# Performance work log

Measured on AMD Instinct MI355X. Metric: run time of the kernel, lower is better.

The kernel has to match this reference:

```python
import jax, jax.numpy as jnp
import numpy as np

N = 2048
D_T = 256; D_F = 256
E_T = 32; E_F = 32; E_C = 128
C = 5; Q = 512


def setup_inputs() -> dict:
    key = jax.random.key(0)
    ks = jax.random.split(key, 12)
    # full graph minus self-loops, row-major (matches dense_to_sparse ordering)
    r, c = np.meshgrid(np.arange(N), np.arange(N), indexing='ij')
    m = r != c
    edge_index = jnp.asarray(np.stack([r[m], c[m]]), dtype=jnp.int32)  # [2, N*(N-1)]
    E = edge_index.shape[1]
    s = 0.02
    return {
        'time_features': jax.random.normal(ks[0], (N, D_T), jnp.float32),
        'edge_index': edge_index,
        'time_edge_weight': jax.random.uniform(ks[1], (E,), jnp.float32),
        'freq_features': jax.random.normal(ks[2], (N, D_F), jnp.float32),
        'freq_edge_weight': jax.random.uniform(ks[3], (E,), jnp.float32),
        'labels': jax.random.randint(ks[4], (N,), 0, C, jnp.int32),
        'num_classes': C,
        'query_size': Q,
        'Wt': jax.random.normal(ks[5], (D_T, E_T), jnp.float32) * s,
        'bt': jnp.zeros((E_T,), jnp.float32),
        'Wf': jax.random.normal(ks[6], (D_F, E_F), jnp.float32) * s,
        'bf': jnp.zeros((E_F,), jnp.float32),
        'Wc': jax.random.normal(ks[7], (E_T + E_F + C, E_C), jnp.float32) * s,
        'bc': jnp.zeros((E_C,), jnp.float32),
        'Wo': jax.random.normal(ks[8], (E_C, C), jnp.float32) * s,
        'bo': jnp.zeros((C,), jnp.float32),
    }


def _gcn(x, A, W, b):
    # torch_geometric GCNConv: D^{-1/2}(A + I)D^{-1/2} (X W) + b
    n = A.shape[0]
    Ah = A + jnp.eye(n, dtype=A.dtype)
    deg = Ah.sum(axis=1)
    dis = jnp.where(deg > 0, jax.lax.rsqrt(deg), 0.0)
    return (dis[:, None] * Ah * dis[None, :]) @ (x @ W) + b


def reference(time_features, edge_index, time_edge_weight, freq_features,
              freq_edge_weight, labels, num_classes, query_size,
              Wt, bt, Wf, bf, Wc, bc, Wo, bo):
    n = time_features.shape[0]
    lrelu = lambda z: jax.nn.leaky_relu(z, 0.01)

    def dense_adj(w):  # A[dst, src] = w
        return jnp.zeros((n, n), w.dtype).at[edge_index[1], edge_index[0]].add(w)

    te = lrelu(_gcn(time_features, dense_adj(time_edge_weight), Wt, bt))
    fe = lrelu(_gcn(freq_features, dense_adj(freq_edge_weight), Wf, bf))

    # to_one_hot: one_hot[:n - query_size, labels] = 1 -> support rows get 1 in
    # every column that appears anywhere in `labels`
    cols = jnp.zeros((num_classes,), te.dtype).at[labels].set(1.0)
    rowmask = (jnp.arange(n) < (n - query_size)).astype(te.dtype)
    one_hot = rowmask[:, None] * cols[None, :]

    feats = jnp.concatenate([te, fe, one_hot], axis=-1)  # [n, E_T+E_F+C]

    # graph_construction (no_grad in original): 1 / (L1 distance over the
    # non-one-hot dims + 1e-5), zero diagonal
    fd = jax.lax.stop_gradient(feats[:, : feats.shape[1] - num_classes])
    dist = jnp.sum(jnp.abs(fd[:, None, :] - fd[None, :, :]), axis=-1)  # [n, n]
    Aw = (1.0 / (dist + 1e-5)) * (1.0 - jnp.eye(n, dtype=feats.dtype))

    emb = lrelu(_gcn(feats, Aw, Wc, bc))
    return emb @ Wo + bo
```

## Files before the change

kernel.cpp:

```cpp
#include <hip/hip_runtime.h>
#include <hip/hip_bf16.h>

#define N 2048
#define NM1 2047
#define DT 256
#define ET 32
#define EC 128
#define NC 5
#define FS 80
#define FD 69
#define KC_ET 16
#define KC_EC 16

typedef __hip_bfloat16 bf16;

__global__ __launch_bounds__(256) void k_deg_label(const float* __restrict__ tw,
                                                   const float* __restrict__ fw,
                                                   const int* __restrict__ labels,
                                                   float* __restrict__ degT,
                                                   float* __restrict__ degF,
                                                   float* __restrict__ cols){
    int b = blockIdx.x;
    int t = threadIdx.x;
    if (b == 512){
        __shared__ float lc[NC];
        if (t < NC) lc[t] = 0.f;
        __syncthreads();
        for (int i = t; i < N; i += 256){
            int l = labels[i];
            if (l >= 0 && l < NC) lc[l] = 1.f;
        }
        __syncthreads();
        if (t < NC) cols[t] = lc[t];
        return;
    }
    int p = (b & 7)*256 + t;
    if (p >= NM1) return;
    int s0 = (b >> 3)*32;
    float lowT=0.f, highT=0.f, lowF=0.f, highF=0.f;
    #pragma unroll 8
    for (int r = 0; r < 32; ++r){
        int s = s0 + r;
        float vt = tw[(size_t)s*NM1 + p];
        float vf = fw[(size_t)s*NM1 + p];
        if (s <= p){ highT += vt; highF += vf; }
        else       { lowT  += vt; lowF  += vf; }
    }
    atomicAdd(&degT[p],   lowT);
    atomicAdd(&degF[p],   lowF);
    atomicAdd(&degT[p+1], highT);
    atomicAdd(&degF[p+1], highF);
}

__global__ __launch_bounds__(256) void k_xw2(const float* __restrict__ Xt,
                                             const float* __restrict__ Wt,
                                             const float* __restrict__ degT,
                                             float* __restrict__ Zt,
                                             const float* __restrict__ Xf,
                                             const float* __restrict__ Wf,
                                             const float* __restrict__ degF,
                                             float* __restrict__ Zf){
    const float* X   = blockIdx.y ? Xf   : Xt;
    const float* W   = blockIdx.y ? Wf   : Wt;
    const float* deg = blockIdx.y ? degF : degT;
    float*       Z   = blockIdx.y ? Zf   : Zt;
    __shared__ float Ws[DT*ET];
    __shared__ float Xs[8*DT];
    int t = threadIdx.x;
    for (int idx = t; idx < DT*ET; idx += 256) Ws[idx] = W[idx];
    int i0 = blockIdx.x*8;
    for (int idx = t; idx < 8*DT; idx += 256) Xs[idx] = X[(size_t)i0*DT + idx];
    __syncthreads();
    int r = t >> 5, f = t & 31;
    const float* xr = Xs + r*DT;
    float acc = 0.f;
    #pragma unroll 8
    for (int d = 0; d < DT; ++d) acc += xr[d]*Ws[d*ET+f];
    int i = i0 + r;
    Z[(size_t)i*ET+f] = rsqrtf(1.f + deg[i])*acc;
}

__global__ __launch_bounds__(128) void k_agg_et(const float* __restrict__ tw,
                                                const float* __restrict__ fw,
                                                const float* __restrict__ Zt,
                                                const float* __restrict__ Zf,
                                                float* __restrict__ Pt,
                                                float* __restrict__ Pf){
    __shared__ float Ast[64*68];
    __shared__ float Asf[64*68];
    __shared__ float Zst[64*ET];
    __shared__ float Zsf[64*ET];
    int t = threadIdx.x;
    int i0 = blockIdx.x*64;
    int kc = blockIdx.y;
    int k0 = kc*128;
    int rowg = t >> 3;
    int colth = t & 7;
    int r0 = rowg*4, c0 = colth*4;
    float accT[4][4], accF[4][4];
    #pragma unroll
    for (int u=0;u<4;++u)
        #pragma unroll
        for (int v=0;v<4;++v){ accT[u][v]=0.f; accF[u][v]=0.f; }

    for (int kt = 0; kt < 2; ++kt){
        int kb = k0 + kt*64;
        #pragma unroll
        for (int e = 0; e < 32; ++e){
            int id = t + e*128;
            int k_l = id >> 6, i_l = id & 63;
            int k = kb + k_l;
            int gi = i0 + i_l;
            float vt, vf;
            if (gi == k){ vt = 0.f; vf = 0.f; }
            else {
                size_t base = (size_t)k*NM1 + gi - (gi > k ? 1 : 0);
                vt = tw[base]; vf = fw[base];
            }
            Ast[k_l*68 + i_l] = vt;
            Asf[k_l*68 + i_l] = vf;
        }
        #pragma unroll
        for (int e = 0; e < 4; ++e){
            int id = t + e*128;
            int row = id >> 3;
            int c4  = (id & 7)*4;
            *(float4*)&Zst[row*ET + c4] = *(const float4*)&Zt[(size_t)(kb+row)*ET + c4];
            *(float4*)&Zsf[row*ET + c4] = *(const float4*)&Zf[(size_t)(kb+row)*ET + c4];
        }
        __syncthreads();
        for (int k = 0; k < 64; ++k){
            float4 at = *(const float4*)&Ast[k*68 + r0];
            float4 af = *(const float4*)&Asf[k*68 + r0];
            float4 zt = *(const float4*)&Zst[k*ET + c0];
            float4 zf = *(const float4*)&Zsf[k*ET + c0];
            const float* ap = (const float*)&at;
            const float* bp = (const float*)&af;
            const float* zp = (const float*)&zt;
            const float* wp = (const float*)&zf;
            #pragma unroll
            for (int u = 0; u < 4; ++u)
                #pragma unroll
                for (int v = 0; v < 4; ++v){
                    accT[u][v] += ap[u]*zp[v];
                    accF[u][v] += bp[u]*wp[v];
                }
        }
        __syncthreads();
    }
    #pragma unroll
    for (int u = 0; u < 4; ++u){
        size_t ii = (size_t)(i0 + r0 + u);
        float4 ot, of;
        float* pt = (float*)&ot; float* pf = (float*)&of;
        #pragma unroll
        for (int v = 0; v < 4; ++v){ pt[v]=accT[u][v]; pf[v]=accF[u][v]; }
        *(float4*)&Pt[(size_t)kc*(N*ET) + ii*ET + c0] = ot;
        *(float4*)&Pf[(size_t)kc*(N*ET) + ii*ET + c0] = of;
    }
}

__global__ __launch_bounds__(256) void k_feats_epi(const float* __restrict__ Pt,
                                                   const float* __restrict__ Pf,
                                                   const float* __restrict__ Zt,
                                                   const float* __restrict__ Zf,
                                                   const float* __restrict__ degT,
                                                   const float* __restrict__ degF,
                                                   const float* __restrict__ bt,
                                                   const float* __restrict__ bfv,
                                                   const float* __restrict__ cols,
                                                   const int* __restrict__ qsize,
                                                   float* __restrict__ feats){
    int idx = blockIdx.x*256 + threadIdx.x;
    int i = idx >> 6;
    int f = idx & 63;
    float s, rd, b;
    if (f < ET){
        s = Zt[(size_t)i*ET + f];
        #pragma unroll
        for (int kc = 0; kc < KC_ET; ++kc) s += Pt[(size_t)kc*(N*ET) + (size_t)i*ET + f];
        rd = rsqrtf(1.f + degT[i]);
        b = bt[f];
    } else {
        int g = f - ET;
        s = Zf[(size_t)i*ET + g];
        #pragma unroll
        for (int kc = 0; kc < KC_ET; ++kc) s += Pf[(size_t)kc*(N*ET) + (size_t)i*ET + g];
        rd = rsqrtf(1.f + degF[i]);
        b = bfv[g];
    }
    float v = rd*s + b;
    feats[(size_t)i*FS + f] = v > 0.f ? v : 0.01f*v;
    if (f < NC){
        int nsup = N - qsize[0];
        feats[(size_t)i*FS + 2*ET + f] = (i < nsup) ? cols[f] : 0.f;
    }
}

__global__ __launch_bounds__(256) void k_build_aw(const float* __restrict__ feats,
                                                  float* __restrict__ Aw,
                                                  float* __restrict__ dsum){
    __shared__ float fiT[64*68];
    __shared__ float fjT[64*68];
    int t = threadIdx.x;
    int i0 = blockIdx.x*64, j0 = blockIdx.y*64;
    {
        int row = t >> 2;
        int cb  = (t & 3)*16;
        const float4* si = (const float4*)(feats + (size_t)(i0+row)*FS + cb);
        const float4* sj = (const float4*)(feats + (size_t)(j0+row)*FS + cb);
        #pragma unroll
        for (int s = 0; s < 4; ++s){
            float4 v = si[s];
            float4 w = sj[s];
            int c = cb + s*4;
            fiT[(c+0)*68+row]=v.x; fiT[(c+1)*68+row]=v.y; fiT[(c+2)*68+row]=v.z; fiT[(c+3)*68+row]=v.w;
            fjT[(c+0)*68+row]=w.x; fjT[(c+1)*68+row]=w.y; fjT[(c+2)*68+row]=w.z; fjT[(c+3)*68+row]=w.w;
        }
    }
    __syncthreads();
    int tx = t & 15, ty = t >> 4;
    float acc[4][4];
    #pragma unroll
    for (int u=0;u<4;++u)
        #pragma unroll
        for (int v=0;v<4;++v) acc[u][v]=0.f;
    for (int d = 0; d < 64; ++d){
        float4 a4 = *(const float4*)&fiT[d*68 + ty*4];
        float4 b4 = *(const float4*)&fjT[d*68 + tx*4];
        const float* ap = (const float*)&a4;
        const float* bp = (const float*)&b4;
        #pragma unroll
        for (int u = 0; u < 4; ++u)
            #pragma unroll
            for (int v = 0; v < 4; ++v)
                acc[u][v] += fabsf(ap[u]-bp[v]);
    }
    #pragma unroll
    for (int u = 0; u < 4; ++u){
        int gi = i0 + ty*4 + u;
        float4 o;
        float* po = (float*)&o;
        #pragma unroll
        for (int v = 0; v < 4; ++v){
            int gj = j0 + tx*4 + v;
            po[v] = (gi==gj) ? 1.0f : 1.0f/(acc[u][v] + 1e-5f);
        }
        *(float4*)&Aw[(size_t)gi*N + j0 + tx*4] = o;
        float rs = (po[0]+po[1]) + (po[2]+po[3]);
        rs += __shfl_xor(rs, 1);
        rs += __shfl_xor(rs, 2);
        rs += __shfl_xor(rs, 4);
        rs += __shfl_xor(rs, 8);
        if (tx == 0) atomicAdd(&dsum[gi], rs);
    }
}

__global__ __launch_bounds__(256) void k_featswc(const float* __restrict__ feats,
                                                 const float* __restrict__ Wc,
                                                 const float* __restrict__ dsum,
                                                 float* __restrict__ Zc){
    __shared__ float Wcs[FD*EC];
    __shared__ float fr[8][FD+3];
    int t = threadIdx.x;
    for (int idx = t; idx < FD*EC; idx += 256) Wcs[idx] = Wc[idx];
    int i0 = blockIdx.x*8;
    for (int idx = t; idx < 8*FD; idx += 256){
        int r = idx / FD;
        int c = idx - r*FD;
        fr[r][c] = feats[(size_t)(i0+r)*FS + c];
    }
    __syncthreads();
    int f  = t & 127;
    int rh = t >> 7;
    for (int rr = 0; rr < 4; ++rr){
        int r = rh*4 + rr;
        float acc = 0.f;
        #pragma unroll
        for (int d = 0; d < FD; ++d) acc += fr[r][d]*Wcs[d*EC+f];
        int i = i0 + r;
        Zc[(size_t)i*EC + f] = rsqrtf(dsum[i])*acc;
    }
}

__global__ __launch_bounds__(128) void k_agg_ec(const float* __restrict__ Aw,
                                                const float* __restrict__ Zc,
                                                float* __restrict__ Pe){
    __shared__ float AwT[64*68];
    __shared__ float Zs[64*132];
    int t = threadIdx.x;
    int i0 = blockIdx.x*64;
    int kc = blockIdx.y;
    int k0 = kc*128;
    int colth = t & 15, rowg = t >> 4;
    int r0 = rowg*8, c0 = colth*8;
    float acc[8][8];
    #pragma unroll
    for (int u=0;u<8;++u)
        #pragma unroll
        for (int v=0;v<8;++v) acc[u][v]=0.f;

    for (int kt = 0; kt < 2; ++kt){
        int kb = k0 + kt*64;
        #pragma unroll
        for (int e = 0; e < 8; ++e){
            int id = t + e*128;
            int i_l = id >> 4;
            int k4  = (id & 15)*4;
            float4 v = *(const float4*)&Aw[(size_t)(i0+i_l)*N + kb + k4];
            AwT[(k4+0)*68 + i_l] = v.x;
            AwT[(k4+1)*68 + i_l] = v.y;
            AwT[(k4+2)*68 + i_l] = v.z;
            AwT[(k4+3)*68 + i_l] = v.w;
        }
        #pragma unroll
        for (int e = 0; e < 16; ++e){
            int id = t + e*128;
            int row = id >> 5;
            int c4  = (id & 31)*4;
            *(float4*)&Zs[row*132 + c4] = *(const float4*)&Zc[(size_t)(kb+row)*EC + c4];
        }
        __syncthreads();
        for (int k = 0; k < 64; ++k){
            float4 alo = *(const float4*)&AwT[k*68 + r0];
            float4 ahi = *(const float4*)&AwT[k*68 + r0 + 4];
            float4 zlo = *(const float4*)&Zs[k*132 + c0];
            float4 zhi = *(const float4*)&Zs[k*132 + c0 + 4];
            float a8[8] = {alo.x,alo.y,alo.z,alo.w,ahi.x,ahi.y,ahi.z,ahi.w};
            float z8[8] = {zlo.x,zlo.y,zlo.z,zlo.w,zhi.x,zhi.y,zhi.z,zhi.w};
            #pragma unroll
            for (int u = 0; u < 8; ++u)
                #pragma unroll
                for (int v = 0; v < 8; ++v)
                    acc[u][v] += a8[u]*z8[v];
        }
        __syncthreads();
    }
    #pragma unroll
    for (int u = 0; u < 8; ++u){
        size_t ii = (size_t)(i0 + r0 + u);
        float4 o0, o1;
        float* p0 = (float*)&o0; float* p1 = (float*)&o1;
        #pragma unroll
        for (int v = 0; v < 4; ++v){ p0[v]=acc[u][v]; p1[v]=acc[u][v+4]; }
        *(float4*)&Pe[(size_t)kc*(N*EC) + ii*EC + c0]     = o0;
        *(float4*)&Pe[(size_t)kc*(N*EC) + ii*EC + c0 + 4] = o1;
    }
}

__global__ __launch_bounds__(256) void k_emb_epi(const float* __restrict__ Pe,
                                                 const float* __restrict__ dsum,
                                                 const float* __restrict__ bc,
                                                 float* __restrict__ emb){
    int idx = blockIdx.x*256 + threadIdx.x;
    int i = idx >> 7, f = idx & 127;
    float s = 0.f;
    #pragma unroll
    for (int kc = 0; kc < KC_EC; ++kc) s += Pe[(size_t)kc*(N*EC) + (size_t)idx];
    float v = rsqrtf(dsum[i])*s + bc[f];
    emb[idx] = v > 0.f ? v : 0.01f*v;
}

__global__ __launch_bounds__(256) void k_final(const float* __restrict__ emb,
                                               const float* __restrict__ Wo,
                                               const float* __restrict__ bo,
                                               float* __restrict__ out){
    __shared__ float Wos[EC*NC];
    __shared__ float bos[NC];
    int t = threadIdx.x;
    for (int idx = t; idx < EC*NC; idx += 256) Wos[idx] = Wo[idx];
    if (t < NC) bos[t] = bo[t];
    __syncthreads();
    int idx = blockIdx.x*256 + t;
    int i = idx / NC;
    int c = idx - i*NC;
    float acc = bos[c];
    const float* er = emb + (size_t)i*EC;
    #pragma unroll 8
    for (int f = 0; f < EC; ++f) acc += er[f]*Wos[f*NC+c];
    out[idx] = acc;
}

extern "C" void kernel_launch(void* const* d_in, const int* in_sizes, int n_in,
                              void* d_out, int out_size, void* d_ws, size_t ws_size,
                              hipStream_t stream) {
    const float* time_features = (const float*)d_in[0];
    const float* tw            = (const float*)d_in[2];
    const float* freq_features = (const float*)d_in[3];
    const float* fw            = (const float*)d_in[4];
    const int*   labels        = (const int*)d_in[5];
    const int*   qsize         = (const int*)d_in[7];
    const float* Wt  = (const float*)d_in[8];
    const float* bt  = (const float*)d_in[9];
    const float* Wf  = (const float*)d_in[10];
    const float* bfv = (const float*)d_in[11];
    const float* Wc  = (const float*)d_in[12];
    const float* bc  = (const float*)d_in[13];
    const float* Wo  = (const float*)d_in[14];
    const float* bo  = (const float*)d_in[15];
    float* out = (float*)d_out;

    float* ws    = (float*)d_ws;
    float* Zt    = ws;
    float* Zf    = Zt + (size_t)N*ET;
    float* Zc    = Zf + (size_t)N*ET;
    float* degT  = Zc + (size_t)N*EC;
    float* degF  = degT + N;
    float* dsum  = degF + N;
    float* colsb = dsum + N;
    float* feats = colsb + 8;
    float* emb   = feats + (size_t)N*FS;
    float* Aw    = emb + (size_t)N*EC;
    float* Pt    = Aw + (size_t)N*N;
    float* Pf    = Pt + (size_t)KC_ET*N*ET;
    float* Pe    = Pf + (size_t)KC_ET*N*ET;

    hipMemsetAsync(degT, 0, 3*N*sizeof(float), stream);
    k_deg_label<<<513, 256, 0, stream>>>(tw, fw, labels, degT, degF, colsb);
    k_xw2<<<dim3(N/8, 2), 256, 0, stream>>>(time_features, Wt, degT, Zt,
                                            freq_features, Wf, degF, Zf);
    k_agg_et<<<dim3(N/64, KC_ET), 128, 0, stream>>>(tw, fw, Zt, Zf, Pt, Pf);
    k_feats_epi<<<(N*64)/256, 256, 0, stream>>>(Pt, Pf, Zt, Zf, degT, degF,
                                                bt, bfv, colsb, qsize, feats);
    k_build_aw<<<dim3(N/64, N/64), 256, 0, stream>>>(feats, Aw, dsum);
    k_featswc<<<N/8, 256, 0, stream>>>(feats, Wc, dsum, Zc);
    k_agg_ec<<<dim3(N/64, KC_EC), 128, 0, stream>>>(Aw, Zc, Pe);
    k_emb_epi<<<(N*EC)/256, 256, 0, stream>>>(Pe, dsum, bc, emb);
    k_final<<<(N*NC)/256, 256, 0, stream>>>(emb, Wo, bo, out);
}
```

Baseline: 236.6 us.

## Retile graph aggregation GEMMs, use Aw symmetry, fuse embedding epilogue with output

k_agg_et now runs 256 threads per block, with each half computing either the time or the frequency aggregation, which halves per-thread accumulators. k_agg_ec moves to 128-row tiles and 256 threads, and loads Aw rows directly as the K-major tile. Because Aw is symmetric, this removes the scalar transpose scatter into shared memory. The embedding epilogue and the final linear layer are fused into one kernel, which drops the emb buffer and one launch, though only 10 threads per block do the final dot products.

```diff
diff --git a/kernel.cpp b/kernel.cpp
--- a/kernel.cpp
+++ b/kernel.cpp
@@ -80,7 +80,7 @@
     Z[(size_t)i*ET+f] = rsqrtf(1.f + deg[i])*acc;
 }
 
-__global__ __launch_bounds__(128) void k_agg_et(const float* __restrict__ tw,
+__global__ __launch_bounds__(256) void k_agg_et(const float* __restrict__ tw,
                                                 const float* __restrict__ fw,
                                                 const float* __restrict__ Zt,
                                                 const float* __restrict__ Zf,
@@ -94,20 +94,23 @@
     int i0 = blockIdx.x*64;
     int kc = blockIdx.y;
     int k0 = kc*128;
-    int rowg = t >> 3;
-    int colth = t & 7;
-    int r0 = rowg*4, c0 = colth*4;
-    float accT[4][4], accF[4][4];
+    int g  = t >> 7;
+    int tt = t & 127;
+    int ig = tt >> 3, fg = tt & 7;
+    int r0 = ig*4, c0 = fg*4;
+    const float* As = g ? Asf : Ast;
+    const float* Zs = g ? Zsf : Zst;
+    float acc[4][4];
     #pragma unroll
     for (int u=0;u<4;++u)
         #pragma unroll
-        for (int v=0;v<4;++v){ accT[u][v]=0.f; accF[u][v]=0.f; }
+        for (int v=0;v<4;++v) acc[u][v]=0.f;
 
     for (int kt = 0; kt < 2; ++kt){
         int kb = k0 + kt*64;
         #pragma unroll
-        for (int e = 0; e < 32; ++e){
-            int id = t + e*128;
+        for (int e = 0; e < 16; ++e){
+            int id = t + e*256;
             int k_l = id >> 6, i_l = id & 63;
             int k = kb + k_l;
             int gi = i0 + i_l;
@@ -121,8 +124,8 @@
             Asf[k_l*68 + i_l] = vf;
         }
         #pragma unroll
-        for (int e = 0; e < 4; ++e){
-            int id = t + e*128;
+        for (int e = 0; e < 2; ++e){
+            int id = t + e*256;
             int row = id >> 3;
             int c4  = (id & 7)*4;
             *(float4*)&Zst[row*ET + c4] = *(const float4*)&Zt[(size_t)(kb+row)*ET + c4];
@@ -130,33 +133,27 @@
         }
         __syncthreads();
         for (int k = 0; k < 64; ++k){
-            float4 at = *(const float4*)&Ast[k*68 + r0];
-            float4 af = *(const float4*)&Asf[k*68 + r0];
-            float4 zt = *(const float4*)&Zst[k*ET + c0];
-            float4 zf = *(const float4*)&Zsf[k*ET + c0];
-            const float* ap = (const float*)&at;
-            const float* bp = (const float*)&af;
-            const float* zp = (const float*)&zt;
-            const float* wp = (const float*)&zf;
+            float4 a = *(const float4*)&As[k*68 + r0];
+            float4 z = *(const float4*)&Zs[k*ET + c0];
+            const float* ap = (const float*)&a;
+            const float* zp = (const float*)&z;
             #pragma unroll
             for (int u = 0; u < 4; ++u)
                 #pragma unroll
-                for (int v = 0; v < 4; ++v){
-                    accT[u][v] += ap[u]*zp[v];
-                    accF[u][v] += bp[u]*wp[v];
-                }
-        }
-        __syncthreads();
-    }
+                for (int v = 0; v < 4; ++v)
+                    acc[u][v] += ap[u]*zp[v];
+        }
+        __syncthreads();
+    }
+    float* P = g ? Pf : Pt;
     #pragma unroll
     for (int u = 0; u < 4; ++u){
         size_t ii = (size_t)(i0 + r0 + u);
-        float4 ot, of;
-        float* pt = (float*)&ot; float* pf = (float*)&of;
-        #pragma unroll
-        for (int v = 0; v < 4; ++v){ pt[v]=accT[u][v]; pf[v]=accF[u][v]; }
-        *(float4*)&Pt[(size_t)kc*(N*ET) + ii*ET + c0] = ot;
-        *(float4*)&Pf[(size_t)kc*(N*ET) + ii*ET + c0] = of;
+        float4 o;
+        float* po = (float*)&o;
+        #pragma unroll
+        for (int v = 0; v < 4; ++v) po[v]=acc[u][v];
+        *(float4*)&P[(size_t)kc*(N*ET) + ii*ET + c0] = o;
     }
 }
 
@@ -283,17 +280,19 @@
     }
 }
 
-__global__ __launch_bounds__(128) void k_agg_ec(const float* __restrict__ Aw,
+__global__ __launch_bounds__(256) void k_agg_ec(const float* __restrict__ Aw,
                                                 const float* __restrict__ Zc,
                                                 float* __restrict__ Pe){
-    __shared__ float AwT[64*68];
-    __shared__ float Zs[64*132];
-    int t = threadIdx.x;
-    int i0 = blockIdx.x*64;
+    __shared__ float As[64*128];
+    __shared__ float Zs[64*128];
+    int t = threadIdx.x;
+    int i0 = blockIdx.x*128;
     int kc = blockIdx.y;
     int k0 = kc*128;
-    int colth = t & 15, rowg = t >> 4;
-    int r0 = rowg*8, c0 = colth*8;
+    int rg = t >> 4;
+    int cg = t & 15;
+    int r0 = rg*8;
+    int ca = cg*4, cb = 64 + cg*4;
     float acc[8][8];
     #pragma unroll
     for (int u=0;u<8;++u)
@@ -304,35 +303,35 @@
         int kb = k0 + kt*64;
         #pragma unroll
         for (int e = 0; e < 8; ++e){
-            int id = t + e*128;
-            int i_l = id >> 4;
-            int k4  = (id & 15)*4;
-            float4 v = *(const float4*)&Aw[(size_t)(i0+i_l)*N + kb + k4];
-            AwT[(k4+0)*68 + i_l] = v.x;
-            AwT[(k4+1)*68 + i_l] = v.y;
-            AwT[(k4+2)*68 + i_l] = v.z;
-            AwT[(k4+3)*68 + i_l] = v.w;
-        }
-        #pragma unroll
-        for (int e = 0; e < 16; ++e){
-            int id = t + e*128;
+            int id = t + e*256;
+            int k_l = id >> 5;
+            int i4  = (id & 31)*4;
+            *(float4*)&As[k_l*128 + i4] = *(const float4*)&Aw[(size_t)(kb+k_l)*N + i0 + i4];
+        }
+        #pragma unroll
+        for (int e = 0; e < 8; ++e){
+            int id = t + e*256;
             int row = id >> 5;
             int c4  = (id & 31)*4;
-            *(float4*)&Zs[row*132 + c4] = *(const float4*)&Zc[(size_t)(kb+row)*EC + c4];
+            *(float4*)&Zs[row*128 + c4] = *(const float4*)&Zc[(size_t)(kb+row)*EC + c4];
         }
         __syncthreads();
         for (int k = 0; k < 64; ++k){
-            float4 alo = *(const float4*)&AwT[k*68 + r0];
-            float4 ahi = *(const float4*)&AwT[k*68 + r0 + 4];
-            float4 zlo = *(const float4*)&Zs[k*132 + c0];
-            float4 zhi = *(const float4*)&Zs[k*132 + c0 + 4];
-            float a8[8] = {alo.x,alo.y,alo.z,alo.w,ahi.x,ahi.y,ahi.z,ahi.w};
-            float z8[8] = {zlo.x,zlo.y,zlo.z,zlo.w,zhi.x,zhi.y,zhi.z,zhi.w};
+            float4 a0 = *(const float4*)&As[k*128 + r0];
+            float4 a1 = *(const float4*)&As[k*128 + r0 + 4];
+            float4 z0 = *(const float4*)&Zs[k*128 + ca];
+            float4 z1 = *(const float4*)&Zs[k*128 + cb];
+            float a8[8] = {a0.x,a0.y,a0.z,a0.w,a1.x,a1.y,a1.z,a1.w};
+            float zl[4] = {z0.x,z0.y,z0.z,z0.w};
+            float zh[4] = {z1.x,z1.y,z1.z,z1.w};
             #pragma unroll
-            for (int u = 0; u < 8; ++u)
+            for (int u = 0; u < 8; ++u){
                 #pragma unroll
-                for (int v = 0; v < 8; ++v)
-                    acc[u][v] += a8[u]*z8[v];
+                for (int v = 0; v < 4; ++v){
+                    acc[u][v]   += a8[u]*zl[v];
+                    acc[u][v+4] += a8[u]*zh[v];
+                }
+            }
         }
         __syncthreads();
     }
@@ -343,42 +342,40 @@
         float* p0 = (float*)&o0; float* p1 = (float*)&o1;
         #pragma unroll
         for (int v = 0; v < 4; ++v){ p0[v]=acc[u][v]; p1[v]=acc[u][v+4]; }
-        *(float4*)&Pe[(size_t)kc*(N*EC) + ii*EC + c0]     = o0;
-        *(float4*)&Pe[(size_t)kc*(N*EC) + ii*EC + c0 + 4] = o1;
-    }
-}
-
-__global__ __launch_bounds__(256) void k_emb_epi(const float* __restrict__ Pe,
-                                                 const float* __restrict__ dsum,
-                                                 const float* __restrict__ bc,
-                                                 float* __restrict__ emb){
-    int idx = blockIdx.x*256 + threadIdx.x;
-    int i = idx >> 7, f = idx & 127;
-    float s = 0.f;
-    #pragma unroll
-    for (int kc = 0; kc < KC_EC; ++kc) s += Pe[(size_t)kc*(N*EC) + (size_t)idx];
-    float v = rsqrtf(dsum[i])*s + bc[f];
-    emb[idx] = v > 0.f ? v : 0.01f*v;
-}
-
-__global__ __launch_bounds__(256) void k_final(const float* __restrict__ emb,
-                                               const float* __restrict__ Wo,
-                                               const float* __restrict__ bo,
-                                               float* __restrict__ out){
+        *(float4*)&Pe[(size_t)kc*(N*EC) + ii*EC + ca] = o0;
+        *(float4*)&Pe[(size_t)kc*(N*EC) + ii*EC + cb] = o1;
+    }
+}
+
+__global__ __launch_bounds__(256) void k_embfinal(const float* __restrict__ Pe,
+                                                  const float* __restrict__ dsum,
+                                                  const float* __restrict__ bc,
+                                                  const float* __restrict__ Wo,
+                                                  const float* __restrict__ bo,
+                                                  float* __restrict__ out){
+    __shared__ float vs[2][EC];
     __shared__ float Wos[EC*NC];
     __shared__ float bos[NC];
     int t = threadIdx.x;
     for (int idx = t; idx < EC*NC; idx += 256) Wos[idx] = Wo[idx];
     if (t < NC) bos[t] = bo[t];
+    int rr = t >> 7, f = t & 127;
+    int i = blockIdx.x*2 + rr;
+    size_t idx = (size_t)i*EC + f;
+    float s = 0.f;
+    #pragma unroll
+    for (int kc = 0; kc < KC_EC; ++kc) s += Pe[(size_t)kc*(N*EC) + idx];
+    float v = rsqrtf(dsum[i])*s + bc[f];
+    vs[rr][f] = v > 0.f ? v : 0.01f*v;
     __syncthreads();
-    int idx = blockIdx.x*256 + t;
-    int i = idx / NC;
-    int c = idx - i*NC;
-    float acc = bos[c];
-    const float* er = emb + (size_t)i*EC;
-    #pragma unroll 8
-    for (int f = 0; f < EC; ++f) acc += er[f]*Wos[f*NC+c];
-    out[idx] = acc;
+    if (t < 2*NC){
+        int r = t / NC;
+        int c = t - r*NC;
+        float a = bos[c];
+        #pragma unroll 8
+        for (int f2 = 0; f2 < EC; ++f2) a += vs[r][f2]*Wos[f2*NC+c];
+        out[(size_t)(blockIdx.x*2 + r)*NC + c] = a;
+    }
 }
 
 extern "C" void kernel_launch(void* const* d_in, const int* in_sizes, int n_in,
@@ -409,8 +406,7 @@
     float* dsum  = degF + N;
     float* colsb = dsum + N;
     float* feats = colsb + 8;
-    float* emb   = feats + (size_t)N*FS;
-    float* Aw    = emb + (size_t)N*EC;
+    float* Aw    = feats + (size_t)N*FS;
     float* Pt    = Aw + (size_t)N*N;
     float* Pf    = Pt + (size_t)KC_ET*N*ET;
     float* Pe    = Pf + (size_t)KC_ET*N*ET;
@@ -419,12 +415,11 @@
     k_deg_label<<<513, 256, 0, stream>>>(tw, fw, labels, degT, degF, colsb);
     k_xw2<<<dim3(N/8, 2), 256, 0, stream>>>(time_features, Wt, degT, Zt,
                                             freq_features, Wf, degF, Zf);
-    k_agg_et<<<dim3(N/64, KC_ET), 128, 0, stream>>>(tw, fw, Zt, Zf, Pt, Pf);
+    k_agg_et<<<dim3(N/64, KC_ET), 256, 0, stream>>>(tw, fw, Zt, Zf, Pt, Pf);
     k_feats_epi<<<(N*64)/256, 256, 0, stream>>>(Pt, Pf, Zt, Zf, degT, degF,
                                                 bt, bfv, colsb, qsize, feats);
     k_build_aw<<<dim3(N/64, N/64), 256, 0, stream>>>(feats, Aw, dsum);
     k_featswc<<<N/8, 256, 0, stream>>>(feats, Wc, dsum, Zc);
-    k_agg_ec<<<dim3(N/64, KC_EC), 128, 0, stream>>>(Aw, Zc, Pe);
-    k_emb_epi<<<(N*EC)/256, 256, 0, stream>>>(Pe, dsum, bc, emb);
-    k_final<<<(N*NC)/256, 256, 0, stream>>>(emb, Wo, bo, out);
-}
+    k_agg_ec<<<dim3(N/128, KC_EC), 256, 0, stream>>>(Aw, Zc, Pe);
+    k_embfinal<<<N/2, 256, 0, stream>>>(Pe, dsum, bc, Wo, bo, out);
+}
```

After: 212.1 us. 10.4% less time.
